# Kernel tuning notes

Hardware: AMD Instinct MI355X
Metric: run time of the kernel (lower is better)

The kernel has to match this reference:

```python
import jax, jax.numpy as jnp
import numpy as np

N, LH, PL = 512, 20, 10          # agents, history len, prediction len
H, E, NH, FF = 128, 64, 10, 2048  # rnn hidden, embedding, heads, ffn dim
D = H + 2                         # transformer d_model = 130
DH = D // NH                      # head dim = 13
DT = 0.1
NLAYERS = 3


def setup_inputs() -> dict:
    key = jax.random.key(0)
    ks = list(jax.random.split(key, 40))
    def rn(shape, s=0.02):
        return jax.random.normal(ks.pop(), shape, jnp.float32) * s
    Tracks = jax.random.normal(ks.pop(), (N, LH, 5), jnp.float32)
    Tracks = Tracks.at[:, :, 0].set(1.0)  # nonzero ids: all agents active every frame
    return dict(
        Tracks=Tracks,
        W_emb=rn((E, 4)), b_emb=jnp.zeros((E,), jnp.float32),
        W_ih=rn((4 * H, E)), W_hh=rn((4 * H, H)),
        b_ih=jnp.zeros((4 * H,), jnp.float32), b_hh=jnp.zeros((4 * H,), jnp.float32),
        enc_qkv_w=rn((NLAYERS, 3 * D, D)), enc_qkv_b=jnp.zeros((NLAYERS, 3 * D), jnp.float32),
        enc_out_w=rn((NLAYERS, D, D)), enc_out_b=jnp.zeros((NLAYERS, D), jnp.float32),
        enc_ff1_w=rn((NLAYERS, FF, D)), enc_ff1_b=jnp.zeros((NLAYERS, FF), jnp.float32),
        enc_ff2_w=rn((NLAYERS, D, FF)), enc_ff2_b=jnp.zeros((NLAYERS, D), jnp.float32),
        enc_ln1_s=jnp.ones((NLAYERS, D), jnp.float32), enc_ln1_b=jnp.zeros((NLAYERS, D), jnp.float32),
        enc_ln2_s=jnp.ones((NLAYERS, D), jnp.float32), enc_ln2_b=jnp.zeros((NLAYERS, D), jnp.float32),
        W_sp=rn((H, D)), b_sp=jnp.zeros((H,), jnp.float32),
        W_p1=rn((H, H)), b_p1=jnp.zeros((H,), jnp.float32),
        W_p2=rn((H, H)), b_p2=jnp.zeros((H,), jnp.float32),
        W_pl=rn((2, H)), b_pl=jnp.zeros((2,), jnp.float32),
    )


def _ln(x, s, b):
    m = jnp.mean(x, -1, keepdims=True)
    v = jnp.mean((x - m) ** 2, -1, keepdims=True)
    return (x - m) / jnp.sqrt(v + 1e-5) * s + b


def _mha(x, qkv_w, qkv_b, ow, ob):
    # x: [N, D] unbatched sequence of N agent tokens (torch unbatched semantics)
    qkv = x @ qkv_w.T + qkv_b
    q, k, v = jnp.split(qkv, 3, -1)
    def heads(t):
        return t.reshape(-1, NH, DH).transpose(1, 0, 2)  # [NH, N, DH]
    q, k, v = heads(q), heads(k), heads(v)
    scores = jnp.einsum('hnd,hmd->hnm', q, k) / jnp.sqrt(jnp.float32(DH))
    att = jax.nn.softmax(scores, -1)
    o = jnp.einsum('hnm,hmd->hnd', att, v).transpose(1, 0, 2).reshape(-1, D)
    return o @ ow.T + ob


def _forward(Tracks, W_emb, b_emb, W_ih, W_hh, b_ih, b_hh,
             enc_qkv_w, enc_qkv_b, enc_out_w, enc_out_b,
             enc_ff1_w, enc_ff1_b, enc_ff2_w, enc_ff2_b,
             enc_ln1_s, enc_ln1_b, enc_ln2_s, enc_ln2_b,
             W_sp, b_sp, W_p1, b_p1, W_p2, b_p2, W_pl, b_pl):
    def emb(x):
        return x @ W_emb.T + b_emb

    def lstm(x, h, c):  # torch LSTMCell, gate order i,f,g,o
        g = x @ W_ih.T + b_ih + h @ W_hh.T + b_hh
        i, f, gg, o = jnp.split(g, 4, -1)
        c2 = jax.nn.sigmoid(f) * c + jax.nn.sigmoid(i) * jnp.tanh(gg)
        return jax.nn.sigmoid(o) * jnp.tanh(c2), c2

    def sp(h, pos):  # sp_model: 3-layer post-norm transformer encoder + linear
        x = jnp.concatenate([h, pos], 1)  # [N, D]
        for j in range(NLAYERS):
            a = _mha(x, enc_qkv_w[j], enc_qkv_b[j], enc_out_w[j], enc_out_b[j])
            x = _ln(x + a, enc_ln1_s[j], enc_ln1_b[j])
            f = jax.nn.relu(x @ enc_ff1_w[j].T + enc_ff1_b[j]) @ enc_ff2_w[j].T + enc_ff2_b[j]
            x = _ln(x + f, enc_ln2_s[j], enc_ln2_b[j])
        return x @ W_sp.T + b_sp

    def rm_sp(inp, Sh, c):
        h2, c2 = lstm(emb(inp), Sh, c)
        return sp(h2, inp[:, :2]), c2

    n = Tracks.shape[0]
    inp0 = Tracks[:, 0, 1:]
    z = jnp.zeros((n, H), Tracks.dtype)
    h, c = lstm(emb(inp0), z, z)  # step-0 init (original processes step 0 twice)
    Sh = sp(h, inp0[:, :2])

    def step(carry, inp):
        Sh, c = carry
        Sh, c = rm_sp(inp, Sh, c)
        return (Sh, c), None

    (Sh, c), _ = jax.lax.scan(step, (Sh, c), jnp.moveaxis(Tracks[:, :, 1:], 1, 0))

    def pstep(carry, _):
        Sh, c, cf = carry
        x = jax.nn.relu(Sh @ W_p1.T + b_p1) + Sh
        x = jax.nn.relu(x @ W_p2.T + b_p2) + x
        a = x @ W_pl.T + b_pl                       # acceleration [N,2]
        v = a * DT + cf[:, 2:]                      # velocity update first (in-place order)
        pnew = a * (DT * DT / 2) + v * DT + cf[:, :2]
        out = jnp.concatenate([pnew, v], 1)
        Sh, c = rm_sp(out, Sh, c)
        return (Sh, c, out), out

    _, pre = jax.lax.scan(pstep, (Sh, c, Tracks[:, -1, 1:]), None, length=PL)
    return jnp.moveaxis(pre, 0, 1)  # [N, pre_len, 4]


def reference(Tracks, W_emb, b_emb, W_ih, W_hh, b_ih, b_hh,
              enc_qkv_w, enc_qkv_b, enc_out_w, enc_out_b,
              enc_ff1_w, enc_ff1_b, enc_ff2_w, enc_ff2_b,
              enc_ln1_s, enc_ln1_b, enc_ln2_s, enc_ln2_b,
              W_sp, b_sp, W_p1, b_p1, W_p2, b_p2, W_pl, b_pl):
    return _forward(Tracks, W_emb, b_emb, W_ih, W_hh, b_ih, b_hh,
                    enc_qkv_w, enc_qkv_b, enc_out_w, enc_out_b,
                    enc_ff1_w, enc_ff1_b, enc_ff2_w, enc_ff2_b,
                    enc_ln1_s, enc_ln1_b, enc_ln2_s, enc_ln2_b,
                    W_sp, b_sp, W_p1, b_p1, W_p2, b_p2, W_pl, b_pl)
```

## Files before the change

kernel.cpp:

```cpp
#include <hip/hip_runtime.h>


#define Nn 512
#define Dd 130
#define DP 132
#define Hh 128
#define Ee 64
#define FFf 2048
#define KG 192
#define TS 68

typedef float v4 __attribute__((ext_vector_type(4)));
typedef float v2 __attribute__((ext_vector_type(2)));

struct Args {
  const float *Tracks, *W_emb, *b_emb, *W_ih, *W_hh, *b_ih, *b_hh;
  const float *qkv_w, *qkv_b, *out_w, *out_b, *ff1_w, *ff1_b, *ff2_w, *ff2_b;
  const float *ln1_s, *ln1_b, *ln2_s, *ln2_b;
  const float *W_sp, *b_sp, *W_p1, *b_p1, *W_p2, *b_p2, *W_pl, *b_pl;
  float *X, *T, *Q, *Kb, *V, *O, *Sh, *C, *X1, *X2, *Y, *PART, *outp;
};

__device__ __forceinline__ float sigm(float x){ return 1.f/(1.f+__expf(-x)); }

__global__ __launch_bounds__(512) void k_proj(Args a){
  int rg = blockIdx.x & 7, cs = blockIdx.x >> 3;
  int r0 = rg*64, c0 = cs*64;
  __shared__ alignas(16) float xs[Dd*TS];
  __shared__ alignas(16) float ws[Dd*TS];
  int tid = threadIdx.x, cg = tid & 15, ig = tid >> 4;
  for (int idx=tid; idx<64*Dd; idx+=512){ int i=idx/Dd, j=idx-i*Dd; xs[j*TS+i] = a.X[(r0+i)*DP+j]; }
  for (int idx=tid; idx<64*Dd; idx+=512){ int c=idx/Dd, j=idx-c*Dd; ws[j*TS+c] = a.W_sp[(c0+c)*Dd+j]; }
  __syncthreads();
  float acc[2][4] = {};
  const float* xp = xs + 2*ig;
  const float* wp = ws + 4*cg;
  #pragma unroll 4
  for (int j=0;j<Dd;j++){
    v2 xv = *(const v2*)(xp + j*TS);
    v4 wv = *(const v4*)(wp + j*TS);
    #pragma unroll
    for (int aa=0;aa<2;aa++)
      #pragma unroll
      for (int bb=0;bb<4;bb++) acc[aa][bb] += xv[aa]*wv[bb];
  }
  #pragma unroll
  for (int aa=0;aa<2;aa++){
    int r = r0 + 2*ig + aa, c = c0 + 4*cg;
    v4 o; 
    #pragma unroll
    for (int bb=0;bb<4;bb++) o[bb] = acc[aa][bb] + a.b_sp[c+bb];
    *(v4*)&a.Sh[r*Hh+c] = o;
  }
}

__global__ __launch_bounds__(512) void k_mlp(Args a, const float* inp, const float* W, const float* b, float* outp){
  int rg = blockIdx.x & 7, cs = blockIdx.x >> 3;
  int r0 = rg*64, c0 = cs*64;
  __shared__ alignas(16) float xs[Hh*TS];
  __shared__ alignas(16) float ws[Hh*TS];
  int tid = threadIdx.x, cg = tid & 15, ig = tid >> 4;
  for (int idx=tid; idx<64*Hh; idx+=512){ int i=idx>>7, j=idx&127; xs[j*TS+i] = inp[(r0+i)*Hh+j]; }
  for (int idx=tid; idx<64*Hh; idx+=512){ int c=idx>>7, j=idx&127; ws[j*TS+c] = W[(c0+c)*Hh+j]; }
  __syncthreads();
  float acc[2][4] = {};
  const float* xp = xs + 2*ig;
  const float* wp = ws + 4*cg;
  #pragma unroll 4
  for (int j=0;j<Hh;j++){
    v2 xv = *(const v2*)(xp + j*TS);
    v4 wv = *(const v4*)(wp + j*TS);
    #pragma unroll
    for (int aa=0;aa<2;aa++)
      #pragma unroll
      for (int bb=0;bb<4;bb++) acc[aa][bb] += xv[aa]*wv[bb];
  }
  #pragma unroll
  for (int aa=0;aa<2;aa++){
    int r = r0 + 2*ig + aa, c = c0 + 4*cg;
    v4 ri = *(const v4*)&inp[r*Hh+c];
    v4 o;
    #pragma unroll
    for (int bb=0;bb<4;bb++) o[bb] = fmaxf(acc[aa][bb]+b[c+bb],0.f) + ri[bb];
    *(v4*)&outp[r*Hh+c] = o;
  }
}

__global__ __launch_bounds__(256) void k_pout(Args a, int p){
  int r0 = blockIdx.x*8;
  __shared__ float red[16*17];
  int tid = threadIdx.x;
  int o = tid & 15, kq = tid >> 4;
  int ii = o>>1, jj = o&1, r = r0+ii;
  float s = 0.f;
  for (int v=kq*8; v<kq*8+8; v++) s += a.X2[r*Hh+v]*a.W_pl[jj*Hh+v];
  red[o*17+kq] = s;
  __syncthreads();
  if (tid < 16){
    int oo=tid, i2=oo>>1, j=oo&1, rr=r0+i2;
    float av = a.b_pl[j];
    for (int k=0;k<16;k++) av += red[oo*17+k];
    float cf0, cf2;
    if (p==0){ cf0 = a.Tracks[(rr*20+19)*5+1+j]; cf2 = a.Tracks[(rr*20+19)*5+3+j]; }
    else     { cf0 = a.outp[rr*40+(p-1)*4+j];    cf2 = a.outp[rr*40+(p-1)*4+2+j]; }
    float vv = av*0.1f + cf2;
    float pn = av*0.005f + vv*0.1f + cf0;
    a.outp[rr*40+p*4+j]   = pn;
    a.outp[rr*40+p*4+2+j] = vv;
  }
}

__global__ __launch_bounds__(512) void k_gates(Args a, int xin_mode, int tstep, int p, int sh_zero){
  int rg = blockIdx.x & 7, us = blockIdx.x >> 3;
  int r0 = rg*64, u0 = us*16;
  __shared__ alignas(16) float xs[KG*TS];
  __shared__ alignas(16) float ws[KG*TS];
  __shared__ float xin[64*4];
  int tid = threadIdx.x, cg = tid & 15, ig = tid >> 4;
  for (int idx=tid; idx<64*4; idx+=512){ int i=idx>>2, j=idx&3; int r=r0+i;
    xin[i*4+j] = (xin_mode==0) ? a.Tracks[(r*20+tstep)*5+1+j] : a.outp[r*40+p*4+j]; }
  for (int idx=tid; idx<64*Hh; idx+=512){ int i=idx>>7, v=idx&127;
    xs[(Ee+v)*TS+i] = sh_zero ? 0.f : a.Sh[(r0+i)*Hh+v]; }
  for (int idx=tid; idx<64*KG; idx+=512){ int row=idx/KG, j=idx-row*KG;
    int u=row>>2, g=row&3; int wrow = g*Hh + u0 + u;
    ws[j*TS+row] = (j<Ee) ? a.W_ih[wrow*Ee+j] : a.W_hh[wrow*Hh+(j-Ee)]; }
  __syncthreads();
  for (int idx=tid; idx<64*Ee; idx+=512){ int e=idx>>6, i=idx&63;
    float s = a.b_emb[e];
    #pragma unroll
    for (int j=0;j<4;j++) s += xin[i*4+j]*a.W_emb[e*4+j];
    xs[e*TS+i] = s; }
  __syncthreads();
  float acc[2][4] = {};
  const float* xp = xs + 2*ig;
  const float* wp = ws + 4*cg;
  #pragma unroll 4
  for (int j=0;j<KG;j++){
    v2 xv = *(const v2*)(xp + j*TS);
    v4 wv = *(const v4*)(wp + j*TS);
    #pragma unroll
    for (int aa=0;aa<2;aa++)
      #pragma unroll
      for (int bb=0;bb<4;bb++) acc[aa][bb] += xv[aa]*wv[bb];
  }
  int u = u0 + cg;
  #pragma unroll
  for (int rr=0;rr<2;rr++){
    int r = r0 + 2*ig + rr;
    float gi = acc[rr][0] + a.b_ih[u]      + a.b_hh[u];
    float gf = acc[rr][1] + a.b_ih[Hh+u]   + a.b_hh[Hh+u];
    float gg = acc[rr][2] + a.b_ih[2*Hh+u] + a.b_hh[2*Hh+u];
    float go = acc[rr][3] + a.b_ih[3*Hh+u] + a.b_hh[3*Hh+u];
    float cp = sh_zero ? 0.f : a.C[r*Hh+u];
    float c2 = sigm(gf)*cp + sigm(gi)*tanhf(gg);
    a.C[r*Hh+u] = c2;
    a.X[r*DP+u] = sigm(go)*tanhf(c2);
  }
  if (us==0 && tid<128){ int i=tid>>1, jj=tid&1;
    a.X[(r0+i)*DP + Hh + jj] = xin[i*4+jj]; }
}

__global__ __launch_bounds__(512) void k_qkv(Args a, int layer){
  int rg = blockIdx.x & 7, cs = blockIdx.x >> 3;
  int r0 = rg*64, c0 = cs*64;
  __shared__ alignas(16) float xs[Dd*TS];
  __shared__ alignas(16) float ws[Dd*TS];
  const float* qw = a.qkv_w + layer*390*Dd;
  const float* qb = a.qkv_b + layer*390;
  int tid = threadIdx.x, cg = tid & 15, ig = tid >> 4;
  for (int idx=tid; idx<64*Dd; idx+=512){ int i=idx/Dd, j=idx-i*Dd; xs[j*TS+i] = a.X[(r0+i)*DP+j]; }
  for (int idx=tid; idx<64*Dd; idx+=512){ int c=idx/Dd, j=idx-c*Dd; int gc=c0+c;
    ws[j*TS+c] = (gc<390) ? qw[gc*Dd+j] : 0.f; }
  __syncthreads();
  float acc[2][4] = {};
  const float* xp = xs + 2*ig;
  const float* wp = ws + 4*cg;
  #pragma unroll 4
  for (int j=0;j<Dd;j++){
    v2 xv = *(const v2*)(xp + j*TS);
    v4 wv = *(const v4*)(wp + j*TS);
    #pragma unroll
    for (int aa=0;aa<2;aa++)
      #pragma unroll
      for (int bb=0;bb<4;bb++) acc[aa][bb] += xv[aa]*wv[bb];
  }
  #pragma unroll
  for (int aa=0;aa<2;aa++){
    int r = r0 + 2*ig + aa;
    #pragma unroll
    for (int bb=0;bb<4;bb++){
      int c = c0 + 4*cg + bb;
      if (c < 390){
        float v = acc[aa][bb] + qb[c];
        if (c < Dd)        a.Q [r*DP + c]        = v;
        else if (c < 2*Dd) a.Kb[r*DP + (c-Dd)]   = v;
        else               a.V [r*DP + (c-2*Dd)] = v;
      }
    }
  }
}

__global__ __launch_bounds__(256) void k_attn(Args a){
  int rg = blockIdx.x & 31, head = blockIdx.x >> 5;
  int r0 = rg*16, hc = head*13;
  __shared__ alignas(16) float kv[512*14];
  __shared__ alignas(16) float sc[16*516];
  __shared__ float red[16*17];
  __shared__ float rowm[16], rowsi[16];
  int tid = threadIdx.x;
  const float scale = rsqrtf(13.f);
  for (int idx=tid; idx<512*13; idx+=256){ int m=idx/13, d=idx-13*m; kv[m*14+d]=a.Kb[m*DP+hc+d]; }
  __syncthreads();
  { int ii=tid>>4, mg=tid&15;
    float q[13];
    #pragma unroll
    for (int d=0;d<13;d++) q[d]=a.Q[(r0+ii)*DP+hc+d]*scale;
    for (int k=0;k<32;k++){ int m=mg+16*k;
      float s=0.f;
      #pragma unroll
      for (int d=0;d<13;d++) s += q[d]*kv[m*14+d];
      sc[ii*516+m]=s; } }
  __syncthreads();
  for (int idx=tid; idx<512*13; idx+=256){ int m=idx/13, d=idx-13*m; kv[d*524+m]=a.V[m*DP+hc+d]; }
  { int row=tid>>4, l=tid&15; float mx=-1e30f;
    for (int k=0;k<32;k++) mx=fmaxf(mx, sc[row*516+l+16*k]);
    red[row*17+l]=mx; }
  __syncthreads();
  if (tid<16){ float mx=-1e30f; for(int k=0;k<16;k++) mx=fmaxf(mx,red[tid*17+k]); rowm[tid]=mx; }
  __syncthreads();
  { int row=tid>>4, l=tid&15; float s=0.f; float mx=rowm[row];
    for (int k=0;k<32;k++){ int m=l+16*k; float e=__expf(sc[row*516+m]-mx); sc[row*516+m]=e; s+=e; }
    red[row*17+l]=s; }
  __syncthreads();
  if (tid<16){ float s=0.f; for(int k=0;k<16;k++) s+=red[tid*17+k]; rowsi[tid]=1.f/s; }
  __syncthreads();
  if (tid<208){ int ii=tid/13, d=tid-13*ii;
    float accv=0.f;
    const float* sp = sc + ii*516;
    const float* vp = kv + d*524;
    #pragma unroll 4
    for (int mb=0;mb<128;mb++){
      v4 sv = *(const v4*)(sp + 4*mb);
      v4 vv = *(const v4*)(vp + 4*mb);
      accv += sv[0]*vv[0]+sv[1]*vv[1]+sv[2]*vv[2]+sv[3]*vv[3];
    }
    a.O[(r0+ii)*DP+hc+d]=accv*rowsi[ii]; }
}

__global__ __launch_bounds__(512) void k_oproj(Args a, int layer){
  int rg = blockIdx.x & 7, cs = blockIdx.x >> 3;
  int r0 = rg*64, c0 = cs*64;
  __shared__ alignas(16) float xs[Dd*TS];
  __shared__ alignas(16) float ws[Dd*TS];
  const float* ow = a.out_w + layer*Dd*Dd;
  const float* ob = a.out_b + layer*Dd;
  int tid = threadIdx.x, cg = tid & 15, ig = tid >> 4;
  for (int idx=tid; idx<64*Dd; idx+=512){ int i=idx/Dd, j=idx-i*Dd; xs[j*TS+i]=a.O[(r0+i)*DP+j]; }
  for (int idx=tid; idx<64*Dd; idx+=512){ int c=idx/Dd, j=idx-c*Dd; int gc=c0+c;
    ws[j*TS+c] = (gc<Dd) ? ow[gc*Dd+j] : 0.f; }
  __syncthreads();
  float acc[2][4] = {};
  const float* xp = xs + 2*ig;
  const float* wp = ws + 4*cg;
  #pragma unroll 4
  for (int j=0;j<Dd;j++){
    v2 xv = *(const v2*)(xp + j*TS);
    v4 wv = *(const v4*)(wp + j*TS);
    #pragma unroll
    for (int aa=0;aa<2;aa++)
      #pragma unroll
      for (int bb=0;bb<4;bb++) acc[aa][bb] += xv[aa]*wv[bb];
  }
  #pragma unroll
  for (int aa=0;aa<2;aa++){
    int r = r0 + 2*ig + aa;
    #pragma unroll
    for (int bb=0;bb<4;bb++){
      int c = c0 + 4*cg + bb;
      if (c < Dd) a.T[r*DP+c] = acc[aa][bb] + ob[c] + a.X[r*DP+c];
    }
  }
}

__global__ __launch_bounds__(256) void k_ln(Args a, const float* s, const float* b, int mode_ff, int layer){
  int r0 = blockIdx.x*8;
  __shared__ float row[8*132];
  __shared__ float red1[8*33], red2[8*33];
  __shared__ float mu[8], inv[8];
  int tid = threadIdx.x, i = tid>>5, l = tid&31;
  if (mode_ff==0){
    for (int idx=tid; idx<8*Dd; idx+=256){ int ii=idx/Dd, c=idx-ii*Dd; row[ii*132+c]=a.T[(r0+ii)*DP+c]; }
  } else {
    const float* f2b = a.ff2_b + layer*Dd;
    for (int idx=tid; idx<8*Dd; idx+=256){ int ii=idx/Dd, c=idx-ii*Dd;
      float sum = a.X[(r0+ii)*DP+c] + f2b[c];
      for (int ksl=0;ksl<16;ksl++) sum += a.PART[(ksl*Nn + r0+ii)*DP + c];
      row[ii*132+c]=sum; }
  }
  __syncthreads();
  { float s1=0.f, s2=0.f;
    for (int k=0;k<5;k++){ int c=l+32*k; if(c<Dd){ float v=row[i*132+c]; s1+=v; s2+=v*v; } }
    red1[i*33+l]=s1; red2[i*33+l]=s2; }
  __syncthreads();
  if (tid<8){ float s1=0.f,s2=0.f; for(int k=0;k<32;k++){ s1+=red1[tid*33+k]; s2+=red2[tid*33+k]; }
    float m=s1/130.f; mu[tid]=m; inv[tid]=rsqrtf(s2/130.f - m*m + 1e-5f); }
  __syncthreads();
  for (int idx=tid; idx<8*Dd; idx+=256){ int ii=idx/Dd, c=idx-ii*Dd;
    a.X[(r0+ii)*DP+c] = (row[ii*132+c]-mu[ii])*inv[ii]*s[c] + b[c]; }
}

__global__ __launch_bounds__(512) void k_ff1(Args a, int layer){
  int rg = blockIdx.x & 7, cs = blockIdx.x >> 3;
  int r0 = rg*64, c0 = cs*64;
  __shared__ alignas(16) float xs[Dd*TS];
  __shared__ alignas(16) float ws[Dd*TS];
  const float* w1 = a.ff1_w + layer*FFf*Dd;
  const float* b1 = a.ff1_b + layer*FFf;
  int tid = threadIdx.x, cg = tid & 15, ig = tid >> 4;
  for (int idx=tid; idx<64*Dd; idx+=512){ int i=idx/Dd, j=idx-i*Dd; xs[j*TS+i]=a.X[(r0+i)*DP+j]; }
  for (int idx=tid; idx<64*Dd; idx+=512){ int c=idx/Dd, j=idx-c*Dd; ws[j*TS+c]=w1[(c0+c)*Dd+j]; }
  __syncthreads();
  float acc[2][4] = {};
  const float* xp = xs + 2*ig;
  const float* wp = ws + 4*cg;
  #pragma unroll 4
  for (int j=0;j<Dd;j++){
    v2 xv = *(const v2*)(xp + j*TS);
    v4 wv = *(const v4*)(wp + j*TS);
    #pragma unroll
    for (int aa=0;aa<2;aa++)
      #pragma unroll
      for (int bb=0;bb<4;bb++) acc[aa][bb] += xv[aa]*wv[bb];
  }
  #pragma unroll
  for (int aa=0;aa<2;aa++){
    int r = r0 + 2*ig + aa, c = c0 + 4*cg;
    v4 o;
    #pragma unroll
    for (int bb=0;bb<4;bb++) o[bb] = fmaxf(acc[aa][bb]+b1[c+bb],0.f);
    *(v4*)&a.Y[r*FFf+c] = o;
  }
}

__global__ __launch_bounds__(512) void k_ff2(Args a, int layer){
  int b = blockIdx.x;
  int rg = b & 7; int t = b >> 3; int ks = t/3; int cs = t - ks*3;
  int r0 = rg*64, c0 = cs*64, k0 = ks*128;
  __shared__ alignas(16) float xs[128*TS];
  __shared__ alignas(16) float ws[128*TS];
  const float* w2 = a.ff2_w + layer*Dd*FFf;
  int tid = threadIdx.x, cg = tid & 15, ig = tid >> 4;
  for (int idx=tid; idx<64*128; idx+=512){ int i=idx>>7, j=idx&127; xs[j*TS+i]=a.Y[(r0+i)*FFf+k0+j]; }
  for (int idx=tid; idx<64*128; idx+=512){ int c=idx>>7, j=idx&127; int gc=c0+c;
    ws[j*TS+c] = (gc<Dd) ? w2[gc*FFf+k0+j] : 0.f; }
  __syncthreads();
  float acc[2][4] = {};
  const float* xp = xs + 2*ig;
  const float* wp = ws + 4*cg;
  #pragma unroll 4
  for (int j=0;j<128;j++){
    v2 xv = *(const v2*)(xp + j*TS);
    v4 wv = *(const v4*)(wp + j*TS);
    #pragma unroll
    for (int aa=0;aa<2;aa++)
      #pragma unroll
      for (int bb=0;bb<4;bb++) acc[aa][bb] += xv[aa]*wv[bb];
  }
  #pragma unroll
  for (int aa=0;aa<2;aa++){
    int r = r0 + 2*ig + aa;
    #pragma unroll
    for (int bb=0;bb<4;bb++){
      int c = c0 + 4*cg + bb;
      if (c < Dd) a.PART[(ks*Nn + r)*DP + c] = acc[aa][bb];
    }
  }
}

extern "C" void kernel_launch(void* const* d_in, const int* in_sizes, int n_in,
                              void* d_out, int out_size, void* d_ws, size_t ws_size,
                              hipStream_t stream) {
  (void)in_sizes; (void)n_in; (void)out_size; (void)ws_size;
  Args A;
  const float* const* in = (const float* const*)d_in;
  A.Tracks=in[0]; A.W_emb=in[1]; A.b_emb=in[2]; A.W_ih=in[3]; A.W_hh=in[4]; A.b_ih=in[5]; A.b_hh=in[6];
  A.qkv_w=in[7]; A.qkv_b=in[8]; A.out_w=in[9]; A.out_b=in[10];
  A.ff1_w=in[11]; A.ff1_b=in[12]; A.ff2_w=in[13]; A.ff2_b=in[14];
  A.ln1_s=in[15]; A.ln1_b=in[16]; A.ln2_s=in[17]; A.ln2_b=in[18];
  A.W_sp=in[19]; A.b_sp=in[20]; A.W_p1=in[21]; A.b_p1=in[22]; A.W_p2=in[23]; A.b_p2=in[24];
  A.W_pl=in[25]; A.b_pl=in[26];
  float* ws = (float*)d_ws;
  A.X   = ws;
  A.T   = ws + 67584;
  A.Q   = ws + 135168;
  A.Kb  = ws + 202752;
  A.V   = ws + 270336;
  A.O   = ws + 337920;
  A.Sh  = ws + 405504;
  A.C   = ws + 471040;
  A.X1  = ws + 536576;
  A.X2  = ws + 602112;
  A.Y   = ws + 667648;
  A.PART= ws + 1716224;
  A.outp = (float*)d_out;

  dim3 B5(512), B2(256);
  auto enc = [&](){
    for (int l=0;l<3;l++){
      k_qkv  <<<dim3(56),  B5, 0, stream>>>(A, l);
      k_attn <<<dim3(320), B2, 0, stream>>>(A);
      k_oproj<<<dim3(24),  B5, 0, stream>>>(A, l);
      k_ln   <<<dim3(64),  B2, 0, stream>>>(A, A.ln1_s+l*Dd, A.ln1_b+l*Dd, 0, l);
      k_ff1  <<<dim3(256), B5, 0, stream>>>(A, l);
      k_ff2  <<<dim3(384), B5, 0, stream>>>(A, l);
      k_ln   <<<dim3(64),  B2, 0, stream>>>(A, A.ln2_s+l*Dd, A.ln2_b+l*Dd, 1, l);
    }
  };

  k_gates<<<dim3(64), B5, 0, stream>>>(A, 0, 0, 0, 1);
  enc();
  for (int t=0;t<20;t++){
    k_proj <<<dim3(16), B5, 0, stream>>>(A);
    k_gates<<<dim3(64), B5, 0, stream>>>(A, 0, t, 0, 0);
    enc();
  }
  for (int p=0;p<10;p++){
    k_proj<<<dim3(16), B5, 0, stream>>>(A);
    k_mlp <<<dim3(16), B5, 0, stream>>>(A, A.Sh, A.W_p1, A.b_p1, A.X1);
    k_mlp <<<dim3(16), B5, 0, stream>>>(A, A.X1, A.W_p2, A.b_p2, A.X2);
    k_pout<<<dim3(64), B2, 0, stream>>>(A, p);
    if (p < 9){
      k_gates<<<dim3(64), B5, 0, stream>>>(A, 1, 0, p, 0);
      enc();
    }
  }
}
```

Baseline: 9.059 ms.

## Fuse final LN with projection/MLP/output head and widen GEMM register tiles

Adds a boundary kernel that fuses the last encoder layer-norm, the spatial projection, both prediction MLP layers and the output head into one launch. This replaces k_ln, k_proj, two k_mlp and k_pout at each step, removing launches and intermediate global round-trips. All GEMM kernels switch to a 4x4 per-thread register tile computed by only 256 of 512 threads. ff2 now splits K into 8 chunks instead of 16, halving the partial-sum buffers. Idle threads and fewer blocks may lower occupancy and parallelism in exchange for fewer launches and better register reuse.

```diff
diff --git a/kernel.cpp b/kernel.cpp
--- a/kernel.cpp
+++ b/kernel.cpp
@@ -7,7 +7,6 @@
 #define Hh 128
 #define Ee 64
 #define FFf 2048
-#define KG 192
 #define TS 68
 
 typedef float v4 __attribute__((ext_vector_type(4)));
@@ -18,143 +17,68 @@
   const float *qkv_w, *qkv_b, *out_w, *out_b, *ff1_w, *ff1_b, *ff2_w, *ff2_b;
   const float *ln1_s, *ln1_b, *ln2_s, *ln2_b;
   const float *W_sp, *b_sp, *W_p1, *b_p1, *W_p2, *b_p2, *W_pl, *b_pl;
-  float *X, *T, *Q, *Kb, *V, *O, *Sh, *C, *X1, *X2, *Y, *PART, *outp;
+  float *X, *T, *Q, *Kb, *V, *O, *Sh, *C, *Y, *PART, *outp;
 };
 
 __device__ __forceinline__ float sigm(float x){ return 1.f/(1.f+__expf(-x)); }
 
-__global__ __launch_bounds__(512) void k_proj(Args a){
-  int rg = blockIdx.x & 7, cs = blockIdx.x >> 3;
-  int r0 = rg*64, c0 = cs*64;
-  __shared__ alignas(16) float xs[Dd*TS];
-  __shared__ alignas(16) float ws[Dd*TS];
-  int tid = threadIdx.x, cg = tid & 15, ig = tid >> 4;
-  for (int idx=tid; idx<64*Dd; idx+=512){ int i=idx/Dd, j=idx-i*Dd; xs[j*TS+i] = a.X[(r0+i)*DP+j]; }
-  for (int idx=tid; idx<64*Dd; idx+=512){ int c=idx/Dd, j=idx-c*Dd; ws[j*TS+c] = a.W_sp[(c0+c)*Dd+j]; }
-  __syncthreads();
-  float acc[2][4] = {};
-  const float* xp = xs + 2*ig;
-  const float* wp = ws + 4*cg;
-  #pragma unroll 4
-  for (int j=0;j<Dd;j++){
-    v2 xv = *(const v2*)(xp + j*TS);
-    v4 wv = *(const v4*)(wp + j*TS);
-    #pragma unroll
-    for (int aa=0;aa<2;aa++)
-      #pragma unroll
-      for (int bb=0;bb<4;bb++) acc[aa][bb] += xv[aa]*wv[bb];
-  }
-  #pragma unroll
-  for (int aa=0;aa<2;aa++){
-    int r = r0 + 2*ig + aa, c = c0 + 4*cg;
-    v4 o; 
-    #pragma unroll
-    for (int bb=0;bb<4;bb++) o[bb] = acc[aa][bb] + a.b_sp[c+bb];
-    *(v4*)&a.Sh[r*Hh+c] = o;
-  }
-}
-
-__global__ __launch_bounds__(512) void k_mlp(Args a, const float* inp, const float* W, const float* b, float* outp){
-  int rg = blockIdx.x & 7, cs = blockIdx.x >> 3;
-  int r0 = rg*64, c0 = cs*64;
-  __shared__ alignas(16) float xs[Hh*TS];
-  __shared__ alignas(16) float ws[Hh*TS];
-  int tid = threadIdx.x, cg = tid & 15, ig = tid >> 4;
-  for (int idx=tid; idx<64*Hh; idx+=512){ int i=idx>>7, j=idx&127; xs[j*TS+i] = inp[(r0+i)*Hh+j]; }
-  for (int idx=tid; idx<64*Hh; idx+=512){ int c=idx>>7, j=idx&127; ws[j*TS+c] = W[(c0+c)*Hh+j]; }
-  __syncthreads();
-  float acc[2][4] = {};
-  const float* xp = xs + 2*ig;
-  const float* wp = ws + 4*cg;
-  #pragma unroll 4
-  for (int j=0;j<Hh;j++){
-    v2 xv = *(const v2*)(xp + j*TS);
-    v4 wv = *(const v4*)(wp + j*TS);
-    #pragma unroll
-    for (int aa=0;aa<2;aa++)
-      #pragma unroll
-      for (int bb=0;bb<4;bb++) acc[aa][bb] += xv[aa]*wv[bb];
-  }
-  #pragma unroll
-  for (int aa=0;aa<2;aa++){
-    int r = r0 + 2*ig + aa, c = c0 + 4*cg;
-    v4 ri = *(const v4*)&inp[r*Hh+c];
-    v4 o;
-    #pragma unroll
-    for (int bb=0;bb<4;bb++) o[bb] = fmaxf(acc[aa][bb]+b[c+bb],0.f) + ri[bb];
-    *(v4*)&outp[r*Hh+c] = o;
-  }
-}
-
-__global__ __launch_bounds__(256) void k_pout(Args a, int p){
-  int r0 = blockIdx.x*8;
-  __shared__ float red[16*17];
-  int tid = threadIdx.x;
-  int o = tid & 15, kq = tid >> 4;
-  int ii = o>>1, jj = o&1, r = r0+ii;
-  float s = 0.f;
-  for (int v=kq*8; v<kq*8+8; v++) s += a.X2[r*Hh+v]*a.W_pl[jj*Hh+v];
-  red[o*17+kq] = s;
-  __syncthreads();
-  if (tid < 16){
-    int oo=tid, i2=oo>>1, j=oo&1, rr=r0+i2;
-    float av = a.b_pl[j];
-    for (int k=0;k<16;k++) av += red[oo*17+k];
-    float cf0, cf2;
-    if (p==0){ cf0 = a.Tracks[(rr*20+19)*5+1+j]; cf2 = a.Tracks[(rr*20+19)*5+3+j]; }
-    else     { cf0 = a.outp[rr*40+(p-1)*4+j];    cf2 = a.outp[rr*40+(p-1)*4+2+j]; }
-    float vv = av*0.1f + cf2;
-    float pn = av*0.005f + vv*0.1f + cf0;
-    a.outp[rr*40+p*4+j]   = pn;
-    a.outp[rr*40+p*4+2+j] = vv;
-  }
-}
+#define FATCORE(KK) \
+  { const float* xp = xs + 4*ig; \
+    const float* wp = ws + 4*cg; \
+    _Pragma("unroll 2") \
+    for (int j=0;j<(KK);j++){ \
+      v4 xv = *(const v4*)(xp + j*TS); \
+      v4 wv = *(const v4*)(wp + j*TS); \
+      _Pragma("unroll") \
+      for (int aa=0;aa<4;aa++) \
+        _Pragma("unroll") \
+        for (int bb=0;bb<4;bb++) acc[aa][bb] += xv[aa]*wv[bb]; \
+    } }
 
 __global__ __launch_bounds__(512) void k_gates(Args a, int xin_mode, int tstep, int p, int sh_zero){
   int rg = blockIdx.x & 7, us = blockIdx.x >> 3;
   int r0 = rg*64, u0 = us*16;
-  __shared__ alignas(16) float xs[KG*TS];
-  __shared__ alignas(16) float ws[KG*TS];
+  __shared__ alignas(16) float xs[96*TS];
+  __shared__ alignas(16) float ws[96*TS];
   __shared__ float xin[64*4];
-  int tid = threadIdx.x, cg = tid & 15, ig = tid >> 4;
+  int tid = threadIdx.x, cg = tid & 15, ig = (tid>>4) & 15;
   for (int idx=tid; idx<64*4; idx+=512){ int i=idx>>2, j=idx&3; int r=r0+i;
     xin[i*4+j] = (xin_mode==0) ? a.Tracks[(r*20+tstep)*5+1+j] : a.outp[r*40+p*4+j]; }
-  for (int idx=tid; idx<64*Hh; idx+=512){ int i=idx>>7, v=idx&127;
-    xs[(Ee+v)*TS+i] = sh_zero ? 0.f : a.Sh[(r0+i)*Hh+v]; }
-  for (int idx=tid; idx<64*KG; idx+=512){ int row=idx/KG, j=idx-row*KG;
-    int u=row>>2, g=row&3; int wrow = g*Hh + u0 + u;
-    ws[j*TS+row] = (j<Ee) ? a.W_ih[wrow*Ee+j] : a.W_hh[wrow*Hh+(j-Ee)]; }
-  __syncthreads();
-  for (int idx=tid; idx<64*Ee; idx+=512){ int e=idx>>6, i=idx&63;
-    float s = a.b_emb[e];
-    #pragma unroll
-    for (int j=0;j<4;j++) s += xin[i*4+j]*a.W_emb[e*4+j];
-    xs[e*TS+i] = s; }
-  __syncthreads();
-  float acc[2][4] = {};
-  const float* xp = xs + 2*ig;
-  const float* wp = ws + 4*cg;
-  #pragma unroll 4
-  for (int j=0;j<KG;j++){
-    v2 xv = *(const v2*)(xp + j*TS);
-    v4 wv = *(const v4*)(wp + j*TS);
-    #pragma unroll
-    for (int aa=0;aa<2;aa++)
-      #pragma unroll
-      for (int bb=0;bb<4;bb++) acc[aa][bb] += xv[aa]*wv[bb];
-  }
-  int u = u0 + cg;
-  #pragma unroll
-  for (int rr=0;rr<2;rr++){
-    int r = r0 + 2*ig + rr;
-    float gi = acc[rr][0] + a.b_ih[u]      + a.b_hh[u];
-    float gf = acc[rr][1] + a.b_ih[Hh+u]   + a.b_hh[Hh+u];
-    float gg = acc[rr][2] + a.b_ih[2*Hh+u] + a.b_hh[2*Hh+u];
-    float go = acc[rr][3] + a.b_ih[3*Hh+u] + a.b_hh[3*Hh+u];
-    float cp = sh_zero ? 0.f : a.C[r*Hh+u];
-    float c2 = sigm(gf)*cp + sigm(gi)*tanhf(gg);
-    a.C[r*Hh+u] = c2;
-    a.X[r*DP+u] = sigm(go)*tanhf(c2);
+  float acc[4][4] = {};
+  for (int ch=0; ch<2; ch++){
+    __syncthreads();
+    for (int idx=tid; idx<96*64; idx+=512){ int kk=idx>>6, i=idx&63; int k=ch*96+kk;
+      float v;
+      if (k < Ee){
+        v = a.b_emb[k];
+        #pragma unroll
+        for (int j=0;j<4;j++) v += xin[i*4+j]*a.W_emb[k*4+j];
+      } else {
+        v = sh_zero ? 0.f : a.Sh[(r0+i)*Hh + (k-Ee)];
+      }
+      xs[kk*TS+i] = v;
+    }
+    for (int idx=tid; idx<96*64; idx+=512){ int kk=idx>>6, row=idx&63; int k=ch*96+kk;
+      int u=row>>2, g=row&3; int wrow = g*Hh + u0 + u;
+      ws[kk*TS+row] = (k<Ee) ? a.W_ih[wrow*Ee+k] : a.W_hh[wrow*Hh+(k-Ee)];
+    }
+    __syncthreads();
+    if (tid < 256) FATCORE(96)
+  }
+  if (tid < 256){
+    int u = u0 + cg;
+    #pragma unroll
+    for (int aa=0;aa<4;aa++){
+      int r = r0 + 4*ig + aa;
+      float gi = acc[aa][0] + a.b_ih[u]      + a.b_hh[u];
+      float gf = acc[aa][1] + a.b_ih[Hh+u]   + a.b_hh[Hh+u];
+      float gg = acc[aa][2] + a.b_ih[2*Hh+u] + a.b_hh[2*Hh+u];
+      float go = acc[aa][3] + a.b_ih[3*Hh+u] + a.b_hh[3*Hh+u];
+      float cp = sh_zero ? 0.f : a.C[r*Hh+u];
+      float c2 = sigm(gf)*cp + sigm(gi)*tanhf(gg);
+      a.C[r*Hh+u] = c2;
+      a.X[r*DP+u] = sigm(go)*tanhf(c2);
+    }
   }
   if (us==0 && tid<128){ int i=tid>>1, jj=tid&1;
     a.X[(r0+i)*DP + Hh + jj] = xin[i*4+jj]; }
@@ -163,38 +87,30 @@
 __global__ __launch_bounds__(512) void k_qkv(Args a, int layer){
   int rg = blockIdx.x & 7, cs = blockIdx.x >> 3;
   int r0 = rg*64, c0 = cs*64;
-  __shared__ alignas(16) float xs[Dd*TS];
-  __shared__ alignas(16) float ws[Dd*TS];
+  __shared__ alignas(16) float xs[132*TS];
+  __shared__ alignas(16) float ws[132*TS];
   const float* qw = a.qkv_w + layer*390*Dd;
   const float* qb = a.qkv_b + layer*390;
-  int tid = threadIdx.x, cg = tid & 15, ig = tid >> 4;
+  int tid = threadIdx.x, cg = tid & 15, ig = (tid>>4) & 15;
   for (int idx=tid; idx<64*Dd; idx+=512){ int i=idx/Dd, j=idx-i*Dd; xs[j*TS+i] = a.X[(r0+i)*DP+j]; }
   for (int idx=tid; idx<64*Dd; idx+=512){ int c=idx/Dd, j=idx-c*Dd; int gc=c0+c;
     ws[j*TS+c] = (gc<390) ? qw[gc*Dd+j] : 0.f; }
   __syncthreads();
-  float acc[2][4] = {};
-  const float* xp = xs + 2*ig;
-  const float* wp = ws + 4*cg;
-  #pragma unroll 4
-  for (int j=0;j<Dd;j++){
-    v2 xv = *(const v2*)(xp + j*TS);
-    v4 wv = *(const v4*)(wp + j*TS);
-    #pragma unroll
-    for (int aa=0;aa<2;aa++)
-      #pragma unroll
-      for (int bb=0;bb<4;bb++) acc[aa][bb] += xv[aa]*wv[bb];
-  }
-  #pragma unroll
-  for (int aa=0;aa<2;aa++){
-    int r = r0 + 2*ig + aa;
-    #pragma unroll
-    for (int bb=0;bb<4;bb++){
-      int c = c0 + 4*cg + bb;
-      if (c < 390){
-        float v = acc[aa][bb] + qb[c];
-        if (c < Dd)        a.Q [r*DP + c]        = v;
-        else if (c < 2*Dd) a.Kb[r*DP + (c-Dd)]   = v;
-        else               a.V [r*DP + (c-2*Dd)] = v;
+  float acc[4][4] = {};
+  if (tid < 256){
+    FATCORE(Dd)
+    #pragma unroll
+    for (int aa=0;aa<4;aa++){
+      int r = r0 + 4*ig + aa;
+      #pragma unroll
+      for (int bb=0;bb<4;bb++){
+        int c = c0 + 4*cg + bb;
+        if (c < 390){
+          float v = acc[aa][bb] + qb[c];
+          if (c < Dd)        a.Q [r*DP + c]        = v;
+          else if (c < 2*Dd) a.Kb[r*DP + (c-Dd)]   = v;
+          else               a.V [r*DP + (c-2*Dd)] = v;
+        }
       }
     }
   }
@@ -250,34 +166,26 @@
 __global__ __launch_bounds__(512) void k_oproj(Args a, int layer){
   int rg = blockIdx.x & 7, cs = blockIdx.x >> 3;
   int r0 = rg*64, c0 = cs*64;
-  __shared__ alignas(16) float xs[Dd*TS];
-  __shared__ alignas(16) float ws[Dd*TS];
+  __shared__ alignas(16) float xs[132*TS];
+  __shared__ alignas(16) float ws[132*TS];
   const float* ow = a.out_w + layer*Dd*Dd;
   const float* ob = a.out_b + layer*Dd;
-  int tid = threadIdx.x, cg = tid & 15, ig = tid >> 4;
+  int tid = threadIdx.x, cg = tid & 15, ig = (tid>>4) & 15;
   for (int idx=tid; idx<64*Dd; idx+=512){ int i=idx/Dd, j=idx-i*Dd; xs[j*TS+i]=a.O[(r0+i)*DP+j]; }
   for (int idx=tid; idx<64*Dd; idx+=512){ int c=idx/Dd, j=idx-c*Dd; int gc=c0+c;
     ws[j*TS+c] = (gc<Dd) ? ow[gc*Dd+j] : 0.f; }
   __syncthreads();
-  float acc[2][4] = {};
-  const float* xp = xs + 2*ig;
-  const float* wp = ws + 4*cg;
-  #pragma unroll 4
-  for (int j=0;j<Dd;j++){
-    v2 xv = *(const v2*)(xp + j*TS);
-    v4 wv = *(const v4*)(wp + j*TS);
-    #pragma unroll
-    for (int aa=0;aa<2;aa++)
-      #pragma unroll
-      for (int bb=0;bb<4;bb++) acc[aa][bb] += xv[aa]*wv[bb];
-  }
-  #pragma unroll
-  for (int aa=0;aa<2;aa++){
-    int r = r0 + 2*ig + aa;
-    #pragma unroll
-    for (int bb=0;bb<4;bb++){
-      int c = c0 + 4*cg + bb;
-      if (c < Dd) a.T[r*DP+c] = acc[aa][bb] + ob[c] + a.X[r*DP+c];
+  float acc[4][4] = {};
+  if (tid < 256){
+    FATCORE(Dd)
+    #pragma unroll
+    for (int aa=0;aa<4;aa++){
+      int r = r0 + 4*ig + aa;
+      #pragma unroll
+      for (int bb=0;bb<4;bb++){
+        int c = c0 + 4*cg + bb;
+        if (c < Dd) a.T[r*DP+c] = acc[aa][bb] + ob[c] + a.X[r*DP+c];
+      }
     }
   }
 }
@@ -294,7 +202,7 @@
     const float* f2b = a.ff2_b + layer*Dd;
     for (int idx=tid; idx<8*Dd; idx+=256){ int ii=idx/Dd, c=idx-ii*Dd;
       float sum = a.X[(r0+ii)*DP+c] + f2b[c];
-      for (int ksl=0;ksl<16;ksl++) sum += a.PART[(ksl*Nn + r0+ii)*DP + c];
+      for (int ksl=0;ksl<8;ksl++) sum += a.PART[(ksl*Nn + r0+ii)*DP + c];
       row[ii*132+c]=sum; }
   }
   __syncthreads();
@@ -312,68 +220,171 @@
 __global__ __launch_bounds__(512) void k_ff1(Args a, int layer){
   int rg = blockIdx.x & 7, cs = blockIdx.x >> 3;
   int r0 = rg*64, c0 = cs*64;
-  __shared__ alignas(16) float xs[Dd*TS];
-  __shared__ alignas(16) float ws[Dd*TS];
+  __shared__ alignas(16) float xs[132*TS];
+  __shared__ alignas(16) float ws[132*TS];
   const float* w1 = a.ff1_w + layer*FFf*Dd;
   const float* b1 = a.ff1_b + layer*FFf;
-  int tid = threadIdx.x, cg = tid & 15, ig = tid >> 4;
+  int tid = threadIdx.x, cg = tid & 15, ig = (tid>>4) & 15;
   for (int idx=tid; idx<64*Dd; idx+=512){ int i=idx/Dd, j=idx-i*Dd; xs[j*TS+i]=a.X[(r0+i)*DP+j]; }
   for (int idx=tid; idx<64*Dd; idx+=512){ int c=idx/Dd, j=idx-c*Dd; ws[j*TS+c]=w1[(c0+c)*Dd+j]; }
   __syncthreads();
-  float acc[2][4] = {};
-  const float* xp = xs + 2*ig;
-  const float* wp = ws + 4*cg;
-  #pragma unroll 4
-  for (int j=0;j<Dd;j++){
-    v2 xv = *(const v2*)(xp + j*TS);
-    v4 wv = *(const v4*)(wp + j*TS);
-    #pragma unroll
-    for (int aa=0;aa<2;aa++)
-      #pragma unroll
-      for (int bb=0;bb<4;bb++) acc[aa][bb] += xv[aa]*wv[bb];
-  }
-  #pragma unroll
-  for (int aa=0;aa<2;aa++){
-    int r = r0 + 2*ig + aa, c = c0 + 4*cg;
-    v4 o;
-    #pragma unroll
-    for (int bb=0;bb<4;bb++) o[bb] = fmaxf(acc[aa][bb]+b1[c+bb],0.f);
-    *(v4*)&a.Y[r*FFf+c] = o;
+  float acc[4][4] = {};
+  if (tid < 256){
+    FATCORE(Dd)
+    #pragma unroll
+    for (int aa=0;aa<4;aa++){
+      int r = r0 + 4*ig + aa, c = c0 + 4*cg;
+      v4 o;
+      #pragma unroll
+      for (int bb=0;bb<4;bb++) o[bb] = fmaxf(acc[aa][bb]+b1[c+bb],0.f);
+      *(v4*)&a.Y[r*FFf+c] = o;
+    }
   }
 }
 
 __global__ __launch_bounds__(512) void k_ff2(Args a, int layer){
-  int b = blockIdx.x;
-  int rg = b & 7; int t = b >> 3; int ks = t/3; int cs = t - ks*3;
-  int r0 = rg*64, c0 = cs*64, k0 = ks*128;
+  int bidx = blockIdx.x;
+  int rg = bidx & 7; int t = bidx >> 3; int ks = t/3; int cs = t - ks*3;
+  int r0 = rg*64, c0 = cs*64, k0 = ks*256;
   __shared__ alignas(16) float xs[128*TS];
   __shared__ alignas(16) float ws[128*TS];
   const float* w2 = a.ff2_w + layer*Dd*FFf;
-  int tid = threadIdx.x, cg = tid & 15, ig = tid >> 4;
-  for (int idx=tid; idx<64*128; idx+=512){ int i=idx>>7, j=idx&127; xs[j*TS+i]=a.Y[(r0+i)*FFf+k0+j]; }
-  for (int idx=tid; idx<64*128; idx+=512){ int c=idx>>7, j=idx&127; int gc=c0+c;
-    ws[j*TS+c] = (gc<Dd) ? w2[gc*FFf+k0+j] : 0.f; }
-  __syncthreads();
-  float acc[2][4] = {};
-  const float* xp = xs + 2*ig;
-  const float* wp = ws + 4*cg;
-  #pragma unroll 4
-  for (int j=0;j<128;j++){
-    v2 xv = *(const v2*)(xp + j*TS);
-    v4 wv = *(const v4*)(wp + j*TS);
-    #pragma unroll
-    for (int aa=0;aa<2;aa++)
-      #pragma unroll
-      for (int bb=0;bb<4;bb++) acc[aa][bb] += xv[aa]*wv[bb];
-  }
-  #pragma unroll
-  for (int aa=0;aa<2;aa++){
-    int r = r0 + 2*ig + aa;
-    #pragma unroll
-    for (int bb=0;bb<4;bb++){
-      int c = c0 + 4*cg + bb;
-      if (c < Dd) a.PART[(ks*Nn + r)*DP + c] = acc[aa][bb];
-    }
+  int tid = threadIdx.x, cg = tid & 15, ig = (tid>>4) & 15;
+  float acc[4][4] = {};
+  for (int ch=0; ch<2; ch++){
+    __syncthreads();
+    int kb = k0 + ch*128;
+    for (int idx=tid; idx<64*128; idx+=512){ int i=idx>>7, j=idx&127; xs[j*TS+i]=a.Y[(r0+i)*FFf+kb+j]; }
+    for (int idx=tid; idx<64*128; idx+=512){ int c=idx>>7, j=idx&127; int gc=c0+c;
+      ws[j*TS+c] = (gc<Dd) ? w2[gc*FFf+kb+j] : 0.f; }
+    __syncthreads();
+    if (tid < 256) FATCORE(128)
+  }
+  if (tid < 256){
+    #pragma unroll
+    for (int aa=0;aa<4;aa++){
+      int r = r0 + 4*ig + aa;
+      #pragma unroll
+      for (int bb=0;bb<4;bb++){
+        int c = c0 + 4*cg + bb;
+        if (c < Dd) a.PART[(ks*Nn + r)*DP + c] = acc[aa][bb];
+      }
+    }
+  }
+}
+
+__global__ __launch_bounds__(512) void k_bnd(Args a, int do_mlp, int p){
+  int r0 = blockIdx.x*8;
+  __shared__ float row8[8*132];
+  __shared__ float sh8[8*132];
+  __shared__ alignas(16) float xsk[132*12];
+  __shared__ alignas(16) float ws[132*TS];
+  __shared__ float red1[8*33], red2[8*33], mu[8], inv[8];
+  __shared__ float pred_[16*17];
+  int tid = threadIdx.x;
+  const float* f2b = a.ff2_b + 2*Dd;
+  const float* lns = a.ln2_s + 2*Dd;
+  const float* lnb = a.ln2_b + 2*Dd;
+  for (int idx=tid; idx<8*Dd; idx+=512){ int ii=idx/Dd, c=idx-ii*Dd;
+    float sum = a.X[(r0+ii)*DP+c] + f2b[c];
+    for (int ksl=0;ksl<8;ksl++) sum += a.PART[(ksl*Nn + r0+ii)*DP + c];
+    row8[ii*132+c]=sum; }
+  __syncthreads();
+  if (tid<256){ int i=tid>>5, l=tid&31;
+    float s1=0.f, s2=0.f;
+    for (int k=0;k<5;k++){ int c=l+32*k; if(c<Dd){ float v=row8[i*132+c]; s1+=v; s2+=v*v; } }
+    red1[i*33+l]=s1; red2[i*33+l]=s2; }
+  __syncthreads();
+  if (tid<8){ float s1=0.f,s2=0.f; for(int k=0;k<32;k++){ s1+=red1[tid*33+k]; s2+=red2[tid*33+k]; }
+    float m=s1/130.f; mu[tid]=m; inv[tid]=rsqrtf(s2/130.f - m*m + 1e-5f); }
+  __syncthreads();
+  for (int idx=tid; idx<8*Dd; idx+=512){ int ii=idx/Dd, c=idx-ii*Dd;
+    float v = (row8[ii*132+c]-mu[ii])*inv[ii]*lns[c] + lnb[c];
+    a.X[(r0+ii)*DP+c] = v; row8[ii*132+c] = v; }
+  __syncthreads();
+  for (int idx=tid; idx<132*8; idx+=512){ int j=idx>>3, r=idx&7;
+    xsk[j*12+r] = (j<Dd) ? row8[r*132+j] : 0.f; }
+  for (int cc=0; cc<2; cc++){
+    __syncthreads();
+    for (int idx=tid; idx<64*Dd; idx+=512){ int cl=idx/Dd, j=idx-cl*Dd;
+      ws[j*TS+cl] = a.W_sp[(cc*64+cl)*Dd+j]; }
+    __syncthreads();
+    if (tid<64){
+      int ip = tid>>4, cg = tid&15;
+      float acc[2][4] = {};
+      for (int j=0;j<Dd;j++){
+        v2 xv = *(const v2*)(xsk + j*12 + 2*ip);
+        v4 wv = *(const v4*)(ws + j*TS + 4*cg);
+        #pragma unroll
+        for (int aa=0;aa<2;aa++)
+          #pragma unroll
+          for (int bb=0;bb<4;bb++) acc[aa][bb] += xv[aa]*wv[bb];
+      }
+      #pragma unroll
+      for (int aa=0;aa<2;aa++)
+        #pragma unroll
+        for (int bb=0;bb<4;bb++){
+          int r = 2*ip+aa, c = cc*64 + 4*cg + bb;
+          float v = acc[aa][bb] + a.b_sp[c];
+          sh8[r*132+c] = v;
+          a.Sh[(r0+r)*Hh+c] = v;
+        }
+    }
+  }
+  if (!do_mlp) return;
+  for (int m=0;m<2;m++){
+    const float* W  = m ? a.W_p2 : a.W_p1;
+    const float* bi = m ? a.b_p2 : a.b_p1;
+    float* src = m ? row8 : sh8;
+    float* dst = m ? sh8  : row8;
+    __syncthreads();
+    for (int idx=tid; idx<128*8; idx+=512){ int j=idx>>3, r=idx&7; xsk[j*12+r]=src[r*132+j]; }
+    for (int cc=0; cc<2; cc++){
+      __syncthreads();
+      for (int idx=tid; idx<64*Hh; idx+=512){ int cl=idx>>7, j=idx&127;
+        ws[j*TS+cl] = W[(cc*64+cl)*Hh+j]; }
+      __syncthreads();
+      if (tid<64){
+        int ip = tid>>4, cg = tid&15;
+        float acc[2][4] = {};
+        for (int j=0;j<Hh;j++){
+          v2 xv = *(const v2*)(xsk + j*12 + 2*ip);
+          v4 wv = *(const v4*)(ws + j*TS + 4*cg);
+          #pragma unroll
+          for (int aa=0;aa<2;aa++)
+            #pragma unroll
+            for (int bb=0;bb<4;bb++) acc[aa][bb] += xv[aa]*wv[bb];
+        }
+        #pragma unroll
+        for (int aa=0;aa<2;aa++)
+          #pragma unroll
+          for (int bb=0;bb<4;bb++){
+            int r = 2*ip+aa, c = cc*64 + 4*cg + bb;
+            dst[r*132+c] = fmaxf(acc[aa][bb]+bi[c],0.f) + src[r*132+c];
+          }
+      }
+    }
+  }
+  __syncthreads();
+  if (tid < 256){
+    int o = tid & 15, kq = tid >> 4;
+    int ii = o>>1, jj = o&1;
+    float s = 0.f;
+    for (int v=kq*8; v<kq*8+8; v++) s += sh8[ii*132+v]*a.W_pl[jj*Hh+v];
+    pred_[o*17+kq] = s;
+  }
+  __syncthreads();
+  if (tid < 16){
+    int oo=tid, i2=oo>>1, j=oo&1, rr=r0+i2;
+    float av = a.b_pl[j];
+    for (int k=0;k<16;k++) av += pred_[oo*17+k];
+    float cf0, cf2;
+    if (p==0){ cf0 = a.Tracks[(rr*20+19)*5+1+j]; cf2 = a.Tracks[(rr*20+19)*5+3+j]; }
+    else     { cf0 = a.outp[rr*40+(p-1)*4+j];    cf2 = a.outp[rr*40+(p-1)*4+2+j]; }
+    float vv = av*0.1f + cf2;
+    float pn = av*0.005f + vv*0.1f + cf0;
+    a.outp[rr*40+p*4+j]   = pn;
+    a.outp[rr*40+p*4+2+j] = vv;
   }
 }
 
@@ -398,8 +409,6 @@
   A.O   = ws + 337920;
   A.Sh  = ws + 405504;
   A.C   = ws + 471040;
-  A.X1  = ws + 536576;
-  A.X2  = ws + 602112;
   A.Y   = ws + 667648;
   A.PART= ws + 1716224;
   A.outp = (float*)d_out;
@@ -412,26 +421,24 @@
       k_oproj<<<dim3(24),  B5, 0, stream>>>(A, l);
       k_ln   <<<dim3(64),  B2, 0, stream>>>(A, A.ln1_s+l*Dd, A.ln1_b+l*Dd, 0, l);
       k_ff1  <<<dim3(256), B5, 0, stream>>>(A, l);
-      k_ff2  <<<dim3(384), B5, 0, stream>>>(A, l);
-      k_ln   <<<dim3(64),  B2, 0, stream>>>(A, A.ln2_s+l*Dd, A.ln2_b+l*Dd, 1, l);
+      k_ff2  <<<dim3(192), B5, 0, stream>>>(A, l);
+      if (l < 2)
+        k_ln <<<dim3(64),  B2, 0, stream>>>(A, A.ln2_s+l*Dd, A.ln2_b+l*Dd, 1, l);
     }
   };
 
   k_gates<<<dim3(64), B5, 0, stream>>>(A, 0, 0, 0, 1);
-  enc();
-  for (int t=0;t<20;t++){
-    k_proj <<<dim3(16), B5, 0, stream>>>(A);
-    k_gates<<<dim3(64), B5, 0, stream>>>(A, 0, t, 0, 0);
+  for (int pass=0; pass<30; ++pass){
     enc();
-  }
-  for (int p=0;p<10;p++){
-    k_proj<<<dim3(16), B5, 0, stream>>>(A);
-    k_mlp <<<dim3(16), B5, 0, stream>>>(A, A.Sh, A.W_p1, A.b_p1, A.X1);
-    k_mlp <<<dim3(16), B5, 0, stream>>>(A, A.X1, A.W_p2, A.b_p2, A.X2);
-    k_pout<<<dim3(64), B2, 0, stream>>>(A, p);
-    if (p < 9){
+    if (pass < 20){
+      k_bnd  <<<dim3(64), B5, 0, stream>>>(A, 0, 0);
+      k_gates<<<dim3(64), B5, 0, stream>>>(A, 0, pass, 0, 0);
+    } else if (pass < 29){
+      int p = pass - 20;
+      k_bnd  <<<dim3(64), B5, 0, stream>>>(A, 1, p);
       k_gates<<<dim3(64), B5, 0, stream>>>(A, 1, 0, p, 0);
-      enc();
-    }
-  }
-}
+    } else {
+      k_bnd  <<<dim3(64), B5, 0, stream>>>(A, 1, 9);
+    }
+  }
+}
```

Measured after the change: 11.11 ms. 22.6% more time.
